# Kernel tuning notes

Hardware: AMD Instinct MI355X
Metric: run time of the kernel (lower is better)

The kernel has to match this reference:

```python
import jax, jax.numpy as jnp
import numpy as np

EPS = 1e-07

def setup_inputs() -> dict:
    key = jax.random.key(0)
    kx, kw, kb, ku = jax.random.split(key, 4)
    B, S, D, A = 1024, 512, 200, 100
    x = jax.random.normal(kx, (B, S, D), dtype=jnp.float32)
    W = jax.random.normal(kw, (D, A), dtype=jnp.float32)
    b = jax.random.normal(kb, (A,), dtype=jnp.float32)
    u = jax.random.normal(ku, (A, 1), dtype=jnp.float32)
    return {"x": x, "W": W, "b": b, "u": u}

def reference(x, W, b, u):
    # uit: [B,S,A] = tanh(x @ W + b)
    uit = jnp.tanh(jnp.einsum('bsd,da->bsa', x, W) + b)
    # ait: [B,S] raw scores -> exp -> normalize over seq (faithful: no max-subtract)
    ait = jnp.exp(jnp.einsum('bsa,a->bs', uit, u[:, 0]))
    ait = ait / (jnp.sum(ait, axis=1, keepdims=True) + EPS)
    # weighted sum pool over seq: [B,D]
    return jnp.einsum('bsd,bs->bd', x, ait)
```

## Files before the change

kernel.cpp:

```cpp
#include <hip/hip_runtime.h>
#include <math.h>


typedef _Float16 half8 __attribute__((ext_vector_type(8)));
typedef _Float16 half4_ __attribute__((ext_vector_type(4)));
typedef float float4_ __attribute__((ext_vector_type(4)));

#define B_   1024
#define S_   512
#define D_   200
#define A_   100
#define NPAD 128
#define KPAD 224
#define SC   64
#define NCH  (S_ / SC)
#define PITCH_H 232

#define WT_BYTES (NPAD * KPAD * 2)
#define UB_BYTES (NPAD * 2 * 4)
#define NUM_OFF  (WT_BYTES + UB_BYTES)
#define DEN_OFF  (NUM_OFF + (size_t)B_ * NCH * D_ * 4)

__global__ void prep_kernel(const float* __restrict__ W,
                            const float* __restrict__ bias,
                            const float* __restrict__ u,
                            void* __restrict__ ws) {
  _Float16* wt = (_Float16*)ws;
  float* upad = (float*)((char*)ws + WT_BYTES);
  float* bpad = upad + NPAD;
  int idx = blockIdx.x * 256 + threadIdx.x;
  if (idx < NPAD * KPAD) {
    int n = idx / KPAD;
    int k = idx % KPAD;
    float v = (n < A_ && k < D_) ? W[k * A_ + n] : 0.f;
    wt[idx] = (_Float16)v;
  }
  if (blockIdx.x == 0 && threadIdx.x < NPAD) {
    int t = threadIdx.x;
    upad[t] = (t < A_) ? u[t] : 0.f;
    bpad[t] = (t < A_) ? bias[t] : 0.f;
  }
}

__global__ __launch_bounds__(256, 4)
void attn_kernel(const float* __restrict__ x,
                 void* __restrict__ ws) {
  __shared__ _Float16 xs[SC * PITCH_H];
  __shared__ float score_part[4][SC];
  __shared__ float e_lds[SC];

  const int blk  = blockIdx.x;
  const int b    = blk >> 3;
  const int chunk= blk & 7;
  const int tid  = threadIdx.x;
  const int lane = tid & 63;
  const int wave = tid >> 6;
  const int lm   = lane & 15;
  const int lq   = lane >> 4;

  const _Float16* wt = (const _Float16*)ws;
  const float* upad = (const float*)((const char*)ws + WT_BYTES);
  const float* bpad = upad + NPAD;
  float* num_out = (float*)((char*)ws + NUM_OFF);
  float* den_out = (float*)((char*)ws + DEN_OFF);

  half8 Bfrag[2][7];
  float ureg[2], breg[2];
#pragma unroll
  for (int nn = 0; nn < 2; ++nn) {
    int a = (2 * wave + nn) * 16 + lm;
#pragma unroll
    for (int k = 0; k < 7; ++k)
      Bfrag[nn][k] = *(const half8*)(wt + (size_t)a * KPAD + k * 32 + lq * 8);
    ureg[nn] = upad[a];
    breg[nn] = bpad[a];
  }

  {
    int c  = tid & 63;
    int r0 = tid >> 6;
    const float* xg = x + ((size_t)b * S_ + (size_t)chunk * SC) * D_;
#pragma unroll
    for (int j = 0; j < 16; ++j) {
      int row = r0 + 4 * j;
      if (c < 50) {
        float4_ v = *(const float4_*)(xg + row * D_ + c * 4);
        half4_ h = {(_Float16)v.x, (_Float16)v.y, (_Float16)v.z, (_Float16)v.w};
        *(half4_*)(&xs[row * PITCH_H + c * 4]) = h;
      } else if (c < 56) {
        half4_ z = {(_Float16)0.f, (_Float16)0.f, (_Float16)0.f, (_Float16)0.f};
        *(half4_*)(&xs[row * PITCH_H + c * 4]) = z;
      }
    }
  }
  __syncthreads();

  float4_ acc[4][2];
#pragma unroll
  for (int m = 0; m < 4; ++m)
#pragma unroll
    for (int nn = 0; nn < 2; ++nn)
      acc[m][nn] = (float4_){0.f, 0.f, 0.f, 0.f};

#pragma unroll
  for (int k = 0; k < 7; ++k) {
    half8 af[4];
#pragma unroll
    for (int m = 0; m < 4; ++m)
      af[m] = *(const half8*)(&xs[(m * 16 + lm) * PITCH_H + k * 32 + lq * 8]);
#pragma unroll
    for (int m = 0; m < 4; ++m)
#pragma unroll
      for (int nn = 0; nn < 2; ++nn)
        acc[m][nn] = __builtin_amdgcn_mfma_f32_16x16x32_f16(
            af[m], Bfrag[nn][k], acc[m][nn], 0, 0, 0);
  }

  float p[4][4];
#pragma unroll
  for (int m = 0; m < 4; ++m) {
#pragma unroll
    for (int r = 0; r < 4; ++r) {
      float s0 = 0.f;
#pragma unroll
      for (int nn = 0; nn < 2; ++nn) {
        float z  = acc[m][nn][r] + breg[nn];
        float az = fabsf(z);
        float ez = __expf(az + az);
        float rc = __builtin_amdgcn_rcpf(ez + 1.f);
        float t  = fmaf(-2.f, rc, 1.f);
        t = copysignf(t, z);
        s0 = fmaf(t, ureg[nn], s0);
      }
      float v = s0;
      v += __shfl_xor(v, 1);
      v += __shfl_xor(v, 2);
      v += __shfl_xor(v, 4);
      v += __shfl_xor(v, 8);
      p[m][r] = v;
    }
  }
  if (lm == 0) {
#pragma unroll
    for (int m = 0; m < 4; ++m)
#pragma unroll
      for (int r = 0; r < 4; ++r)
        score_part[wave][m * 16 + lq * 4 + r] = p[m][r];
  }
  __syncthreads();

  if (tid < SC) {
    float ssum = score_part[0][tid] + score_part[1][tid] +
                 score_part[2][tid] + score_part[3][tid];
    float e = __expf(ssum);
    e_lds[tid] = e;
    float d = e;
    d += __shfl_xor(d, 1);
    d += __shfl_xor(d, 2);
    d += __shfl_xor(d, 4);
    d += __shfl_xor(d, 8);
    d += __shfl_xor(d, 16);
    d += __shfl_xor(d, 32);
    if (tid == 0) den_out[blk] = d;
  }
  __syncthreads();

  if (tid < D_) {
    float accv = 0.f;
#pragma unroll 4
    for (int s = 0; s < SC; ++s)
      accv = fmaf(e_lds[s], (float)xs[s * PITCH_H + tid], accv);
    num_out[(size_t)blk * D_ + tid] = accv;
  }
}

__global__ __launch_bounds__(256)
void reduce_kernel(const void* __restrict__ ws, float* __restrict__ out) {
  const float* num = (const float*)((const char*)ws + NUM_OFF);
  const float* den = (const float*)((const char*)ws + DEN_OFF);
  int b = blockIdx.x;
  int tid = threadIdx.x;
  if (tid < D_) {
    float s = 0.f, d = 0.f;
#pragma unroll
    for (int c = 0; c < NCH; ++c) {
      s += num[(size_t)(b * NCH + c) * D_ + tid];
      d += den[b * NCH + c];
    }
    out[(size_t)b * D_ + tid] = s / (d + 1e-7f);
  }
}

extern "C" void kernel_launch(void* const* d_in, const int* in_sizes, int n_in,
                              void* d_out, int out_size, void* d_ws, size_t ws_size,
                              hipStream_t stream) {
  const float* x = (const float*)d_in[0];
  const float* W = (const float*)d_in[1];
  const float* b = (const float*)d_in[2];
  const float* u = (const float*)d_in[3];
  float* out = (float*)d_out;

  int prep_elems = NPAD * KPAD;
  int prep_blocks = (prep_elems + 255) / 256;
  prep_kernel<<<prep_blocks, 256, 0, stream>>>(W, b, u, d_ws);
  attn_kernel<<<B_ * NCH, 256, 0, stream>>>(x, d_ws);
  reduce_kernel<<<B_, 256, 0, stream>>>(d_ws, out);
}
```

Measured before the change: 589.6 us.

## Split pooling across all waves, use DPP row reductions, and widen partials

The weighted-sum pooling stage is now spread over all four waves. Each wave covers 16 sequence rows and handles 4 feature columns per lane using half4 loads, where before 200 threads each looped over all 64 rows. Each block now writes four partial numerators, so the workspace and the reduce kernel grow to sum 32 partials per batch. The score reduction switches from shfl_xor to DPP row_shr adds, and the A-fragment loads are interleaved with the MFMAs. The cost is four times more partial-numerator traffic to global memory.

Result: no change. 587.7 us (-0.3%).

```diff
diff --git a/kernel.cpp b/kernel.cpp
--- a/kernel.cpp
+++ b/kernel.cpp
@@ -19,7 +19,11 @@
 #define WT_BYTES (NPAD * KPAD * 2)
 #define UB_BYTES (NPAD * 2 * 4)
 #define NUM_OFF  (WT_BYTES + UB_BYTES)
-#define DEN_OFF  (NUM_OFF + (size_t)B_ * NCH * D_ * 4)
+#define DEN_OFF  (NUM_OFF + (size_t)B_ * NCH * 4 * D_ * 4)
+
+#define DPP_ADD(v, ctrl)                                                     \
+  v += __builtin_bit_cast(float, __builtin_amdgcn_update_dpp(                \
+           0, __builtin_bit_cast(int, v), (ctrl), 0xF, 0xF, true))
 
 __global__ void prep_kernel(const float* __restrict__ W,
                             const float* __restrict__ bias,
@@ -104,24 +108,21 @@
 
 #pragma unroll
   for (int k = 0; k < 7; ++k) {
-    half8 af[4];
-#pragma unroll
-    for (int m = 0; m < 4; ++m)
-      af[m] = *(const half8*)(&xs[(m * 16 + lm) * PITCH_H + k * 32 + lq * 8]);
-#pragma unroll
-    for (int m = 0; m < 4; ++m)
+#pragma unroll
+    for (int m = 0; m < 4; ++m) {
+      half8 af = *(const half8*)(&xs[(m * 16 + lm) * PITCH_H + k * 32 + lq * 8]);
 #pragma unroll
       for (int nn = 0; nn < 2; ++nn)
         acc[m][nn] = __builtin_amdgcn_mfma_f32_16x16x32_f16(
-            af[m], Bfrag[nn][k], acc[m][nn], 0, 0, 0);
-  }
-
-  float p[4][4];
+            af, Bfrag[nn][k], acc[m][nn], 0, 0, 0);
+    }
+  }
+
 #pragma unroll
   for (int m = 0; m < 4; ++m) {
 #pragma unroll
     for (int r = 0; r < 4; ++r) {
-      float s0 = 0.f;
+      float v = 0.f;
 #pragma unroll
       for (int nn = 0; nn < 2; ++nn) {
         float z  = acc[m][nn][r] + breg[nn];
@@ -130,22 +131,14 @@
         float rc = __builtin_amdgcn_rcpf(ez + 1.f);
         float t  = fmaf(-2.f, rc, 1.f);
         t = copysignf(t, z);
-        s0 = fmaf(t, ureg[nn], s0);
+        v = fmaf(t, ureg[nn], v);
       }
-      float v = s0;
-      v += __shfl_xor(v, 1);
-      v += __shfl_xor(v, 2);
-      v += __shfl_xor(v, 4);
-      v += __shfl_xor(v, 8);
-      p[m][r] = v;
-    }
-  }
-  if (lm == 0) {
-#pragma unroll
-    for (int m = 0; m < 4; ++m)
-#pragma unroll
-      for (int r = 0; r < 4; ++r)
-        score_part[wave][m * 16 + lq * 4 + r] = p[m][r];
+      DPP_ADD(v, 0x111);
+      DPP_ADD(v, 0x112);
+      DPP_ADD(v, 0x114);
+      DPP_ADD(v, 0x118);
+      if (lm == 15) score_part[wave][m * 16 + lq * 4 + r] = v;
+    }
   }
   __syncthreads();
 
@@ -165,12 +158,19 @@
   }
   __syncthreads();
 
-  if (tid < D_) {
-    float accv = 0.f;
-#pragma unroll 4
-    for (int s = 0; s < SC; ++s)
-      accv = fmaf(e_lds[s], (float)xs[s * PITCH_H + tid], accv);
-    num_out[(size_t)blk * D_ + tid] = accv;
+  if (lane < 50) {
+    float4_ accv = {0.f, 0.f, 0.f, 0.f};
+#pragma unroll
+    for (int i = 0; i < 16; ++i) {
+      int s = wave * 16 + i;
+      float e = e_lds[s];
+      half4_ h = *(const half4_*)(&xs[s * PITCH_H + lane * 4]);
+      accv.x = fmaf(e, (float)h.x, accv.x);
+      accv.y = fmaf(e, (float)h.y, accv.y);
+      accv.z = fmaf(e, (float)h.z, accv.z);
+      accv.w = fmaf(e, (float)h.w, accv.w);
+    }
+    *(float4_*)(&num_out[((size_t)blk * 4 + wave) * D_ + lane * 4]) = accv;
   }
 }
 
@@ -181,12 +181,13 @@
   int b = blockIdx.x;
   int tid = threadIdx.x;
   if (tid < D_) {
-    float s = 0.f, d = 0.f;
-#pragma unroll
-    for (int c = 0; c < NCH; ++c) {
-      s += num[(size_t)(b * NCH + c) * D_ + tid];
-      d += den[b * NCH + c];
-    }
+    float d = 0.f;
+#pragma unroll
+    for (int c = 0; c < NCH; ++c) d += den[b * NCH + c];
+    float s = 0.f;
+#pragma unroll
+    for (int j = 0; j < NCH * 4; ++j)
+      s += num[((size_t)b * NCH * 4 + j) * D_ + tid];
     out[(size_t)b * D_ + tid] = s / (d + 1e-7f);
   }
 }
```
